# Performance work log

Measured on AMD Instinct MI355X. Metric: run time of the kernel, lower is better.

The kernel has to match this reference:

```python
import jax, jax.numpy as jnp
import numpy as np

B, L, D, DFF, MODES = 16, 1536, 512, 2048, 64
KERNELS = (3, 5, 7)


def setup_inputs() -> dict:
    key = jax.random.key(0)
    ks = jax.random.split(key, 12)
    scale = 1.0 / (D * D)
    f32 = jnp.float32
    return {
        "x": jax.random.normal(ks[0], (B, L, D), f32),
        "w_real": scale * jax.random.normal(ks[1], (D, D, MODES), f32),
        "w_imag": scale * jax.random.normal(ks[2], (D, D, MODES), f32),
        "conv1_w": jax.random.normal(ks[3], (DFF, D), f32) / np.sqrt(D).astype(np.float32),
        "conv2_w": jax.random.normal(ks[4], (D, DFF), f32) / np.sqrt(DFF).astype(np.float32),
        "d1_w1": jax.random.normal(ks[5], (D // 2, D), f32) / np.sqrt(D).astype(np.float32),
        "d1_b1": jnp.zeros((D // 2,), f32),
        "d1_w2": jax.random.normal(ks[6], (len(KERNELS), D // 2), f32) / np.sqrt(D // 2).astype(np.float32),
        "d1_b2": jnp.zeros((len(KERNELS),), f32),
        "d2_w1": jax.random.normal(ks[7], (D // 2, D), f32) / np.sqrt(D).astype(np.float32),
        "d2_b1": jnp.zeros((D // 2,), f32),
        "d2_w2": jax.random.normal(ks[8], (len(KERNELS), D // 2), f32) / np.sqrt(D // 2).astype(np.float32),
        "d2_b2": jnp.zeros((len(KERNELS),), f32),
    }


def _avg_pool1d(x, k):
    # torch AvgPool1d(kernel=k, stride=1, padding=k//2), count_include_pad=True:
    # zero-pad then divide by k everywhere. x: (B, L, D) -> (B, L, D) for odd k.
    pad = k // 2
    xp = jnp.pad(x, ((0, 0), (pad, pad), (0, 0)))
    cs = jnp.pad(jnp.cumsum(xp, axis=1), ((0, 0), (1, 0), (0, 0)))
    return (cs[:, k:, :] - cs[:, :-k, :]) / k


def _moe_decomp(x, w1, b1, w2, b2):
    # trends: (B, L, D, E)
    trends = jnp.stack([_avg_pool1d(x, k) for k in KERNELS], axis=-1)
    h = jax.nn.relu(jnp.einsum("bld,hd->blh", x, w1) + b1)
    logits = jnp.einsum("blh,eh->ble", h, w2) + b2
    gates = jax.nn.softmax(logits, axis=-1)[:, :, None, :]  # (B, L, 1, E)
    x_trend = jnp.sum(trends * gates, axis=-1)
    return x - x_trend  # seasonal component


def _fourier_block(x, w_real, w_imag):
    q_ft = jnp.fft.rfft(x, axis=1)  # (B, L//2+1, D) complex
    modes = min(MODES, q_ft.shape[1])
    weights = (w_real + 1j * w_imag).astype(jnp.complex64)  # (D, D, modes)
    # batched complex matmul over the kept modes (fuses the per-mode loop)
    out_m = jnp.einsum("bmd,dem->bme", q_ft[:, :modes, :], weights[:, :, :modes])
    out_ft = jnp.zeros((x.shape[0], x.shape[1] // 2 + 1, x.shape[2]), jnp.complex64)
    out_ft = out_ft.at[:, :modes, :].set(out_m)
    return jnp.fft.irfft(out_ft, n=x.shape[1], axis=1)


def reference(x, w_real, w_imag, conv1_w, conv2_w,
              d1_w1, d1_b1, d1_w2, d1_b2,
              d2_w1, d2_b1, d2_w2, d2_b2):
    # FEB-f + residual (dropout = identity in eval)
    x = x + _fourier_block(x, w_real, w_imag)
    x = _moe_decomp(x, d1_w1, d1_b1, d1_w2, d1_b2)
    # 1x1 conv FFN == per-token linear layers
    y = jax.nn.relu(jnp.einsum("bld,fd->blf", x, conv1_w))
    y = jnp.einsum("blf,df->bld", y, conv2_w)
    res = _moe_decomp(x + y, d2_w1, d2_b1, d2_w2, d2_b2)
    return res
```

## Files before the change

kernel.cpp:

```cpp
#include <hip/hip_runtime.h>

#define B_   16
#define L_   1536
#define D_   512
#define DFF_ 2048
#define NM   64
#define HID  256

typedef short short8  __attribute__((ext_vector_type(8)));
typedef short short4v __attribute__((ext_vector_type(4)));
typedef float f32x4   __attribute__((ext_vector_type(4)));

__device__ __forceinline__ float b2f(short s) {
  unsigned int u = ((unsigned int)(unsigned short)s) << 16;
  float f; __builtin_memcpy(&f, &u, 4); return f;
}
__device__ __forceinline__ short f2b(float f) {
  unsigned int u; __builtin_memcpy(&u, &f, 4);
  u += 0x7fffu + ((u >> 16) & 1u);
  return (short)(u >> 16);
}
__device__ __forceinline__ f32x4 zero4() {
  f32x4 v; v[0]=0.f; v[1]=0.f; v[2]=0.f; v[3]=0.f; return v;
}

#define MFMA(a,b,c) __builtin_amdgcn_mfma_f32_16x16x32_bf16((a),(b),(c),0,0,0)
#define SWZ(row, grp) (((row) << 6) + ((((grp) ^ ((row) & 7))) << 3))
#define GLDS16(gp, lp) __builtin_amdgcn_global_load_lds( \
    (const __attribute__((address_space(1))) void*)(gp), \
    (__attribute__((address_space(3))) void*)(lp), 16, 0, 0)
#define MEMFENCE asm volatile("" ::: "memory")

__global__ __launch_bounds__(256) void zero_out(float* __restrict__ o, int n) {
  int i = blockIdx.x * 256 + threadIdx.x;
  if (i < n) o[i] = 0.f;
}

__global__ __launch_bounds__(256) void prep_all(
    const float* __restrict__ conv1_w, const float* __restrict__ conv2_w,
    const float* __restrict__ d1_w1,  const float* __restrict__ d2_w1,
    short* __restrict__ c1, short* __restrict__ c2,
    short* __restrict__ dw1, short* __restrict__ dw2,
    short* __restrict__ tcs, short* __restrict__ basis)
{
  int blk = blockIdx.x;
  if (blk < 2304) {
    const float* s; short* d; int i;
    if (blk < 1024)      { s = conv1_w; d = c1;  i = blk * 256 + threadIdx.x; }
    else if (blk < 2048) { s = conv2_w; d = c2;  i = (blk - 1024) * 256 + threadIdx.x; }
    else if (blk < 2176) { s = d1_w1;   d = dw1; i = (blk - 2048) * 256 + threadIdx.x; }
    else                 { s = d2_w1;   d = dw2; i = (blk - 2176) * 256 + threadIdx.x; }
    f32x4 v = ((const f32x4*)s)[i];
    short4v o;
    #pragma unroll
    for (int j = 0; j < 4; ++j) o[j] = f2b(v[j]);
    ((short4v*)d)[i] = o;
    return;
  }
  if (blk < 3072) {
    int i = (blk - 2304) * 256 + threadIdx.x;
    int m = i / L_, l = i - m * L_;
    int mm = (m < 64) ? m : (m - 64);
    int r = (mm * l) % L_;
    float th = (float)r * (6.283185307179586f / (float)L_);
    float s, c; __sincosf(th, &s, &c);
    tcs[i] = f2b((m < 64) ? c : -s);
    return;
  }
  {
    int i = (blk - 3072) * 256 + threadIdx.x;
    int l = i >> 7, k = i & 127;
    int m = (k < 64) ? k : (k - 64);
    int r = (m * l) % L_;
    float th = (float)r * (6.283185307179586f / (float)L_);
    float s, c; __sincosf(th, &s, &c);
    float v = (k < 64) ? ((m == 0) ? 1.f : 2.f) * (1.f / (float)L_) * c
                       : (-2.f / (float)L_) * s;
    basis[i] = f2b(v);
  }
}

__global__ __launch_bounds__(256) void transpose_w(
    const float* __restrict__ wre, const float* __restrict__ wim,
    short* __restrict__ wtr, short* __restrict__ wti)
{
  __shared__ float tile[64][17];
  int dc = blockIdx.x, e = blockIdx.y, t = threadIdx.x;
  int zz = blockIdx.z;
  const float* w = (zz < 4) ? wre : wim;
  short* wt      = (zz < 4) ? wtr : wti;
  int mBase = (zz & 3) * 16;
  {
    int dl = t >> 2, mg = t & 3;
    f32x4 v = *(const f32x4*)(w + ((long)(dc * 64 + dl) * 512 + e) * 64 + mBase + mg * 4);
    tile[dl][mg*4+0] = v[0]; tile[dl][mg*4+1] = v[1];
    tile[dl][mg*4+2] = v[2]; tile[dl][mg*4+3] = v[3];
  }
  __syncthreads();
  if (t < 128) {
    int mr = t >> 3, dg = t & 7;
    short8 o;
    #pragma unroll
    for (int j = 0; j < 8; ++j) o[j] = f2b(tile[dg * 8 + j][mr]);
    *(short8*)(wt + ((long)(mBase + mr) * 512 + e) * 512 + dc * 64 + dg * 8) = o;
  }
}

__global__ __launch_bounds__(256) void transpose_x(const float* __restrict__ x,
                                                   short* __restrict__ xt) {
  __shared__ float tile[64][65];
  int dc = blockIdx.x, lc = blockIdx.y, b = blockIdx.z, t = threadIdx.x;
  const float* xb = x + (long)b * L_ * D_;
  #pragma unroll
  for (int i = 0; i < 4; ++i) {
    int idx = i * 256 + t; int ll = idx >> 4, dg = idx & 15;
    f32x4 v = *(const f32x4*)(xb + (long)(lc * 64 + ll) * D_ + dc * 64 + dg * 4);
    tile[ll][dg*4+0] = v[0]; tile[ll][dg*4+1] = v[1];
    tile[ll][dg*4+2] = v[2]; tile[ll][dg*4+3] = v[3];
  }
  __syncthreads();
  #pragma unroll
  for (int i = 0; i < 2; ++i) {
    int idx = i * 256 + t; int dl = idx >> 3, lg = idx & 7;
    short8 o;
    #pragma unroll
    for (int j = 0; j < 8; ++j) o[j] = f2b(tile[lg * 8 + j][dl]);
    *(short8*)(xt + ((long)b * D_ + dc * 64 + dl) * L_ + lc * 64 + lg * 8) = o;
  }
}

template<bool RELU, bool HASBIAS>
__global__ __launch_bounds__(256) void gemm64(
    const short* __restrict__ A, long ldA,
    const short* __restrict__ W, long ldW,
    const float* __restrict__ bias,
    short* __restrict__ outB, long csr, long csc, int K)
{
  __shared__ short lA[2][64 * 64];
  __shared__ short lW[2][64 * 64];
  const int t = threadIdx.x, lane = t & 63, wid = t >> 6;
  const int quad = lane >> 4, l15 = lane & 15;
  const int wm = (wid & 1) * 32, wn = (wid >> 1) * 32;
  const long row0 = (long)blockIdx.x * 64, col0 = (long)blockIdx.y * 64;
  const short* Ab = A + row0 * ldA;
  const short* Wb = W + col0 * ldW;

  int srcrow[2]; long srcoff[2];
  #pragma unroll
  for (int i = 0; i < 2; ++i) {
    int c = wid * 2 + i;
    int r = c * 8 + (lane >> 3);
    int g = (lane & 7) ^ (r & 7);
    srcrow[i] = r; srcoff[i] = g * 8;
  }

  f32x4 acc[2][2];
  #pragma unroll
  for (int i = 0; i < 2; ++i)
    #pragma unroll
    for (int j = 0; j < 2; ++j) acc[i][j] = zero4();

  const int nk = K >> 6;
  #pragma unroll
  for (int i = 0; i < 2; ++i) {
    int c = wid * 2 + i;
    GLDS16(Ab + (long)srcrow[i] * ldA + srcoff[i], lA[0] + c * 512);
    GLDS16(Wb + (long)srcrow[i] * ldW + srcoff[i], lW[0] + c * 512);
  }
  if (nk > 1) {
    #pragma unroll
    for (int i = 0; i < 2; ++i) {
      int c = wid * 2 + i;
      GLDS16(Ab + (long)srcrow[i] * ldA + 64 + srcoff[i], lA[1] + c * 512);
      GLDS16(Wb + (long)srcrow[i] * ldW + 64 + srcoff[i], lW[1] + c * 512);
    }
  }

  for (int it = 0; it < nk; ++it) {
    if (it + 1 < nk) asm volatile("s_waitcnt vmcnt(4)" ::: "memory");
    else             asm volatile("s_waitcnt vmcnt(0)" ::: "memory");
    __builtin_amdgcn_s_barrier();
    const int cur = it & 1;
    const short* bufA = lA[cur];
    const short* bufW = lW[cur];
    #pragma unroll
    for (int ks = 0; ks < 2; ++ks) {
      int gq = ks * 4 + quad;
      short8 a0 = *(const short8*)&bufA[SWZ(wm + l15, gq)];
      short8 a1 = *(const short8*)&bufA[SWZ(wm + 16 + l15, gq)];
      short8 b0 = *(const short8*)&bufW[SWZ(wn + l15, gq)];
      short8 b1 = *(const short8*)&bufW[SWZ(wn + 16 + l15, gq)];
      acc[0][0] = MFMA(a0, b0, acc[0][0]);
      acc[0][1] = MFMA(a0, b1, acc[0][1]);
      acc[1][0] = MFMA(a1, b0, acc[1][0]);
      acc[1][1] = MFMA(a1, b1, acc[1][1]);
    }
    asm volatile("s_waitcnt lgkmcnt(0)" ::: "memory");
    __builtin_amdgcn_s_barrier();
    const long kn = (long)(it + 2) * 64;
    if (kn < K) {
      #pragma unroll
      for (int i = 0; i < 2; ++i) {
        int c = wid * 2 + i;
        GLDS16(Ab + (long)srcrow[i] * ldA + kn + srcoff[i], lA[cur] + c * 512);
        GLDS16(Wb + (long)srcrow[i] * ldW + kn + srcoff[i], lW[cur] + c * 512);
      }
    }
  }

  #pragma unroll
  for (int ni = 0; ni < 2; ++ni) {
    long col = col0 + wn + ni * 16 + l15;
    float bvv = HASBIAS ? bias[col] : 0.f;
    #pragma unroll
    for (int mi = 0; mi < 2; ++mi) {
      #pragma unroll
      for (int r = 0; r < 4; ++r) {
        long row = row0 + wm + mi * 16 + quad * 4 + r;
        float v = acc[mi][ni][r];
        if (HASBIAS) v += bvv;
        if (RELU)    v = fmaxf(v, 0.f);
        outB[row * csr + col * csc] = f2b(v);
      }
    }
  }
}

template<bool RELU, bool HASBIAS, bool HASRES, bool RESB>
__global__ __launch_bounds__(256) void gemm128(
    const short* __restrict__ A, long ldA, long Az,
    const short* __restrict__ W, long ldW, long Wz,
    const float* __restrict__ bias,
    const void* __restrict__ res, long ldres, long resZ,
    short* __restrict__ outB, long ldC, long Cz, int K)
{
  __shared__ short lA[2][128 * 64];
  __shared__ short lW[2][128 * 64];
  const int t = threadIdx.x, lane = t & 63, wid = t >> 6;
  const int quad = lane >> 4, l15 = lane & 15;
  const int wm = (wid & 1) * 64, wn = (wid >> 1) * 64;
  const long row0 = (long)blockIdx.x * 128, col0 = (long)blockIdx.y * 128;
  const int z = blockIdx.z;
  const short* Ab = A + (long)z * Az + row0 * ldA;
  const short* Wb = W + (long)z * Wz + col0 * ldW;

  int srcrow[4]; long srcoff[4];
  #pragma unroll
  for (int i = 0; i < 4; ++i) {
    int c = wid * 4 + i;
    int r = c * 8 + (lane >> 3);
    int g = (lane & 7) ^ (r & 7);
    srcrow[i] = r; srcoff[i] = g * 8;
  }

  f32x4 acc[4][4];
  #pragma unroll
  for (int i = 0; i < 4; ++i)
    #pragma unroll
    for (int j = 0; j < 4; ++j) acc[i][j] = zero4();

  const int nk = K >> 6;
  #pragma unroll
  for (int i = 0; i < 4; ++i) {
    int c = wid * 4 + i;
    GLDS16(Ab + (long)srcrow[i] * ldA + srcoff[i], lA[0] + c * 512);
    GLDS16(Wb + (long)srcrow[i] * ldW + srcoff[i], lW[0] + c * 512);
  }
  if (nk > 1) {
    #pragma unroll
    for (int i = 0; i < 4; ++i) {
      int c = wid * 4 + i;
      GLDS16(Ab + (long)srcrow[i] * ldA + 64 + srcoff[i], lA[1] + c * 512);
      GLDS16(Wb + (long)srcrow[i] * ldW + 64 + srcoff[i], lW[1] + c * 512);
    }
  }

  for (int it = 0; it < nk; ++it) {
    if (it + 1 < nk) asm volatile("s_waitcnt vmcnt(8)" ::: "memory");
    else             asm volatile("s_waitcnt vmcnt(0)" ::: "memory");
    __builtin_amdgcn_s_barrier();
    const int cur = it & 1;
    const short* bufA = lA[cur];
    const short* bufW = lW[cur];
    #pragma unroll
    for (int ks = 0; ks < 2; ++ks) {
      int gq = ks * 4 + quad;
      short8 av[4], bv[4];
      #pragma unroll
      for (int mi = 0; mi < 4; ++mi) av[mi] = *(const short8*)&bufA[SWZ(wm + mi * 16 + l15, gq)];
      #pragma unroll
      for (int ni = 0; ni < 4; ++ni) bv[ni] = *(const short8*)&bufW[SWZ(wn + ni * 16 + l15, gq)];
      #pragma unroll
      for (int mi = 0; mi < 4; ++mi)
        #pragma unroll
        for (int ni = 0; ni < 4; ++ni)
          acc[mi][ni] = MFMA(av[mi], bv[ni], acc[mi][ni]);
    }
    asm volatile("s_waitcnt lgkmcnt(0)" ::: "memory");
    __builtin_amdgcn_s_barrier();
    const long kn = (long)(it + 2) * 64;
    if (kn < K) {
      #pragma unroll
      for (int i = 0; i < 4; ++i) {
        int c = wid * 4 + i;
        GLDS16(Ab + (long)srcrow[i] * ldA + kn + srcoff[i], lA[cur] + c * 512);
        GLDS16(Wb + (long)srcrow[i] * ldW + kn + srcoff[i], lW[cur] + c * 512);
      }
    }
  }

  #pragma unroll
  for (int ni = 0; ni < 4; ++ni) {
    long col = col0 + wn + ni * 16 + l15;
    float bvv = HASBIAS ? bias[col] : 0.f;
    #pragma unroll
    for (int mi = 0; mi < 4; ++mi) {
      #pragma unroll
      for (int r = 0; r < 4; ++r) {
        long row = row0 + wm + mi * 16 + quad * 4 + r;
        float v = acc[mi][ni][r];
        if (HASBIAS) v += bvv;
        if (RELU)    v = fmaxf(v, 0.f);
        if (HASRES) {
          long ro = (long)z * resZ + row * ldres + col;
          v += RESB ? b2f(((const short*)res)[ro]) : ((const float*)res)[ro];
        }
        outB[(long)z * Cz + row * ldC + col] = f2b(v);
      }
    }
  }
}

template<bool RELU, bool HASRES>
__global__ __launch_bounds__(512, 2) void gemm256(
    const short* __restrict__ A, long ldA,
    const short* __restrict__ W, long ldW,
    const short* __restrict__ res, long ldres,
    short* __restrict__ outB, long ldC, int K, int gn)
{
  __shared__ short sh[65536];
  const int t = threadIdx.x;
  const int lane = t & 63, wid = t >> 6;
  const int quad = lane >> 4, l15 = lane & 15;
  const int wr = wid >> 2, wc = wid & 3;
  const int wch = wc >> 1, cbw = (wc & 1) * 64;

  const int nwg = gridDim.x;
  const int cpx = nwg >> 3;
  const int wg = (blockIdx.x & 7) * cpx + (blockIdx.x >> 3);
  const int bx = wg / gn, by = wg - bx * gn;
  const long row0 = (long)bx * 256, col0 = (long)by * 256;

  const short* Ab = A + row0 * ldA;
  const short* Wb = W + col0 * ldW;

  const int srw = t >> 3;
  const int sg  = (t & 7) ^ (srw & 7);

#define STAGE(TP, KB) do {                                                   \
    const long ko_ = (long)(KB) + sg * 8;                                    \
    _Pragma("unroll")                                                        \
    for (int h_ = 0; h_ < 2; ++h_) {                                         \
      short* dA_ = sh + ((TP) * 2 + h_) * 8192;                              \
      short* dB_ = sh + 32768 + ((TP) * 2 + h_) * 8192;                      \
      _Pragma("unroll")                                                      \
      for (int j_ = 0; j_ < 2; ++j_) {                                       \
        const long gr_ = (long)(h_ * 128 + srw + j_ * 64);                   \
        GLDS16(Ab + gr_ * ldA + ko_, dA_ + (j_ * 512 + t) * 8);              \
        GLDS16(Wb + gr_ * ldW + ko_, dB_ + (j_ * 512 + t) * 8);              \
      }                                                                      \
    }                                                                        \
  } while (0)

  f32x4 acc[8][4];
  #pragma unroll
  for (int i = 0; i < 8; ++i)
    #pragma unroll
    for (int j = 0; j < 4; ++j) acc[i][j] = zero4();

#define PH_LOADS(TP, QM, QN)                                                 \
    const short* aS_ = sh + ((TP) * 2 + wr) * 8192;                          \
    const short* bS_ = sh + 32768 + ((TP) * 2 + wch) * 8192;                 \
    short8 av[4][2], bv[2][2];                                               \
    _Pragma("unroll")                                                        \
    for (int u = 0; u < 4; ++u)                                              \
      _Pragma("unroll")                                                      \
      for (int ks = 0; ks < 2; ++ks)                                         \
        av[u][ks] = *(const short8*)&aS_[SWZ(((QM)*4+u)*16 + l15, ks*4 + quad)]; \
    _Pragma("unroll")                                                        \
    for (int v = 0; v < 2; ++v)                                              \
      _Pragma("unroll")                                                      \
      for (int ks = 0; ks < 2; ++ks)                                         \
        bv[v][ks] = *(const short8*)&bS_[SWZ(cbw + ((QN)*2+v)*16 + l15, ks*4 + quad)];

#define PH_MMA(QM, QN) do {                                                  \
    asm volatile("s_waitcnt lgkmcnt(0)" ::: "memory");                       \
    __builtin_amdgcn_s_setprio(1);                                           \
    _Pragma("unroll")                                                        \
    for (int ks = 0; ks < 2; ++ks)                                           \
      _Pragma("unroll")                                                      \
      for (int u = 0; u < 4; ++u)                                            \
        _Pragma("unroll")                                                    \
        for (int v = 0; v < 2; ++v)                                          \
          acc[(QM)*4+u][(QN)*2+v] =                                          \
              MFMA(av[u][ks], bv[v][ks], acc[(QM)*4+u][(QN)*2+v]);           \
    __builtin_amdgcn_s_setprio(0);                                           \
  } while (0)

#define PH_LEAD(TP, QM, QN) do {                                             \
    PH_LOADS(TP, QM, QN);                                                    \
    PH_MMA(QM, QN);                                                          \
    MEMFENCE; __builtin_amdgcn_s_barrier(); MEMFENCE;                        \
  } while (0)

#define PH_MID(TP, QM, QN) do {                                              \
    PH_LOADS(TP, QM, QN);                                                    \
    MEMFENCE; __builtin_amdgcn_s_barrier();                                  \
    PH_MMA(QM, QN);                                                          \
    MEMFENCE; __builtin_amdgcn_s_barrier(); MEMFENCE;                        \
  } while (0)

  const int NI = K >> 7;
  STAGE(0, 0);

  for (int i = 0; i < NI; ++i) {
    const int kb = i << 7;
    STAGE(1, kb + 64);
    asm volatile("s_waitcnt vmcnt(8)" ::: "memory");
    __builtin_amdgcn_s_barrier(); MEMFENCE;
    PH_LEAD(0, 0, 0);
    PH_MID(0, 1, 0);
    PH_MID(0, 0, 1);
    PH_MID(0, 1, 1);
    if (i + 1 < NI) {
      STAGE(0, kb + 128);
      asm volatile("s_waitcnt vmcnt(8)" ::: "memory");
    } else {
      asm volatile("s_waitcnt vmcnt(0)" ::: "memory");
    }
    __builtin_amdgcn_s_barrier(); MEMFENCE;
    PH_LEAD(1, 0, 0);
    PH_MID(1, 1, 0);
    PH_MID(1, 0, 1);
    PH_MID(1, 1, 1);
  }

  #pragma unroll
  for (int ni = 0; ni < 4; ++ni) {
    long col = col0 + wc * 64 + ni * 16 + l15;
    #pragma unroll
    for (int mi = 0; mi < 8; ++mi) {
      #pragma unroll
      for (int r = 0; r < 4; ++r) {
        long row = row0 + wr * 128 + mi * 16 + quad * 4 + r;
        float v = acc[mi][ni][r];
        if (RELU) v = fmaxf(v, 0.f);
        if (HASRES) v += b2f(res[row * ldres + col]);
        outB[row * ldC + col] = f2b(v);
      }
    }
  }
#undef STAGE
#undef PH_LOADS
#undef PH_MMA
#undef PH_LEAD
#undef PH_MID
}

__global__ __launch_bounds__(256) void mode_gemm(
    const short* __restrict__ qr, const short* __restrict__ qi,
    const short* __restrict__ wr, const short* __restrict__ wi,
    short* __restrict__ outm)
{
  __shared__ short lqr[16 * 64], lqi[16 * 64], lwr[64 * 64], lwi[64 * 64];
  const int m = blockIdx.x, en = blockIdx.y;
  const int t = threadIdx.x, lane = t & 63, wid = t >> 6;
  const int quad = lane >> 4, l15 = lane & 15;
  const short* qrb = qr + (long)m * (B_ * D_);
  const short* qib = qi + (long)m * (B_ * D_);
  const short* wrb = wr + (long)m * (D_ * D_) + (long)en * 64 * D_;
  const short* wib = wi + (long)m * (D_ * D_) + (long)en * 64 * D_;
  f32x4 accr = zero4(), acci = zero4();
  for (int k0 = 0; k0 < D_; k0 += 64) {
    __syncthreads();
    {
      int idx = t & 127; int r = idx >> 3, cg = idx & 7;
      const short* src = (t < 128 ? qrb : qib) + r * D_ + k0 + cg * 8;
      short* dst = (t < 128) ? lqr : lqi;
      *(short8*)&dst[SWZ(r, cg)] = *(const short8*)src;
    }
    #pragma unroll
    for (int i = 0; i < 4; ++i) {
      int idx = i * 256 + t;
      int which = idx >> 9, idx2 = idx & 511;
      int r = idx2 >> 3, cg = idx2 & 7;
      const short* src = (which ? wib : wrb) + r * D_ + k0 + cg * 8;
      short* dst = which ? lwi : lwr;
      *(short8*)&dst[SWZ(r, cg)] = *(const short8*)src;
    }
    __syncthreads();
    #pragma unroll
    for (int ks = 0; ks < 2; ++ks) {
      int gq = ks * 4 + quad;
      short8 ar = *(const short8*)&lqr[SWZ(l15, gq)];
      short8 ai = *(const short8*)&lqi[SWZ(l15, gq)];
      short8 br = *(const short8*)&lwr[SWZ(wid * 16 + l15, gq)];
      short8 bi = *(const short8*)&lwi[SWZ(wid * 16 + l15, gq)];
      short8 nai;
      #pragma unroll
      for (int j = 0; j < 8; ++j) nai[j] = (short)(ai[j] ^ (short)0x8000);
      accr = MFMA(ar, br, accr);
      accr = MFMA(nai, bi, accr);
      acci = MFMA(ar, bi, acci);
      acci = MFMA(ai, br, acci);
    }
  }
  #pragma unroll
  for (int r = 0; r < 4; ++r) {
    int bb = quad * 4 + r;
    long e = (long)en * 64 + wid * 16 + l15;
    long base = ((long)bb * D_ + e) * 128 + m;
    outm[base]      = f2b(accr[r]);
    outm[base + 64] = f2b(acci[r]);
  }
}

template<bool OUTF, bool WRITEB>
__global__ __launch_bounds__(512) void combine_kernel(
    const short* __restrict__ xin, const short* __restrict__ h,
    const float* __restrict__ w2, const float* __restrict__ b2,
    float* __restrict__ outf, short* __restrict__ outb)
{
  __shared__ float lG[64][4];
  int lc = blockIdx.x, b = blockIdx.y, t = threadIdx.x;
  int wid = t >> 6, lane = t & 63;
  int l0 = lc * 64;
  #pragma unroll
  for (int pi = 0; pi < 8; ++pi) {
    int pos = wid * 8 + pi;
    long row = (long)b * L_ + l0 + pos;
    short4v hh = *(const short4v*)(h + row * HID + lane * 4);
    float hv[4];
    #pragma unroll
    for (int j = 0; j < 4; ++j) hv[j] = b2f(hh[j]);
    float lg[3];
    #pragma unroll
    for (int e = 0; e < 3; ++e) {
      const float* wrow = w2 + e * HID + lane * 4;
      float p = hv[0] * wrow[0] + hv[1] * wrow[1] + hv[2] * wrow[2] + hv[3] * wrow[3];
      #pragma unroll
      for (int off = 32; off >= 1; off >>= 1) p += __shfl_xor(p, off);
      lg[e] = p + b2[e];
    }
    float mx = fmaxf(lg[0], fmaxf(lg[1], lg[2]));
    float e0 = __expf(lg[0] - mx), e1 = __expf(lg[1] - mx), e2 = __expf(lg[2] - mx);
    float inv = 1.f / (e0 + e1 + e2);
    float gv = (lane == 0) ? e0 * inv : (lane == 1) ? e1 * inv : e2 * inv;
    if (lane < 3) lG[pos][lane] = gv;
  }
  __syncthreads();

  int d = t;
  const short* xb = xin + (long)b * L_ * D_ + d;
  float win[7];
  #pragma unroll
  for (int j = 0; j < 6; ++j) {
    int l = l0 - 3 + j;
    win[j] = (l >= 0 && l < L_) ? b2f(xb[(long)l * D_]) : 0.f;
  }
  for (int i = 0; i < 64; ++i) {
    int lcn = l0 + i;
    int lr = lcn + 3;
    win[6] = (lr < L_) ? b2f(xb[(long)lr * D_]) : 0.f;
    float s3 = win[2] + win[3] + win[4];
    float s5 = s3 + win[1] + win[5];
    float s7 = s5 + win[0] + win[6];
    float trend = lG[i][0] * s3 * (1.f / 3.f) + lG[i][1] * s5 * (1.f / 5.f)
                + lG[i][2] * s7 * (1.f / 7.f);
    float v = win[3] - trend;
    long o = ((long)b * L_ + lcn) * D_ + d;
    if (OUTF)   outf[o] = v;
    if (WRITEB) outb[o] = f2b(v);
    #pragma unroll
    for (int j = 0; j < 6; ++j) win[j] = win[j + 1];
  }
}

extern "C" void kernel_launch(void* const* d_in, const int* in_sizes, int n_in,
                              void* d_out, int out_size, void* d_ws, size_t ws_size,
                              hipStream_t stream) {
  const float* x       = (const float*)d_in[0];
  const float* w_real  = (const float*)d_in[1];
  const float* w_imag  = (const float*)d_in[2];
  const float* conv1_w = (const float*)d_in[3];
  const float* conv2_w = (const float*)d_in[4];
  const float* d1_w1   = (const float*)d_in[5];
  const float* d1_b1   = (const float*)d_in[6];
  const float* d1_w2   = (const float*)d_in[7];
  const float* d1_b2   = (const float*)d_in[8];
  const float* d2_w1   = (const float*)d_in[9];
  const float* d2_b1   = (const float*)d_in[10];
  const float* d2_w2   = (const float*)d_in[11];
  const float* d2_b2   = (const float*)d_in[12];
  float* OUT = (float*)d_out;

  const size_t REQ_BIG = 144703488, REQ_SMALL = 98566144;
  if (ws_size < REQ_SMALL) {
    zero_out<<<(out_size + 255) / 256, 256, 0, stream>>>(OUT, out_size);
    return;
  }
  const bool big = (ws_size >= REQ_BIG);

  char* ws = (char*)d_ws;
  short* C1WB  = (short*)(ws + 0);
  short* C2WB  = (short*)(ws + 2097152);
  short* D1W1B = (short*)(ws + 4194304);
  short* D2W1B = (short*)(ws + 4456448);
  short* TCS   = (short*)(ws + 4718592);
  short* BASIS = (short*)(ws + 5111808);
  short* XT    = (short*)(ws + 6291456);
  short* Y1    = XT;
  short* QRI   = (short*)(ws + 31457280);
  short* OUTM  = (short*)(ws + 33554432);
  short* WTR   = (short*)(ws + 35651584);
  short* X1B   = WTR;
  short* WTI   = (short*)(ws + 69206016);
  short* X2B   = (short*)(ws + (big ? 106954752 : 60817408));
  short* H     = (short*)(ws + (big ? 132120576 : 85983232));

  prep_all<<<3840, 256, 0, stream>>>(conv1_w, conv2_w, d1_w1, d2_w1,
                                     C1WB, C2WB, D1W1B, D2W1B, TCS, BASIS);
  transpose_w<<<dim3(8, 512, 8), 256, 0, stream>>>(w_real, w_imag, WTR, WTI);
  transpose_x<<<dim3(8, 24, 16), 256, 0, stream>>>(x, XT);

  gemm64<false, false><<<dim3(128, 2), 256, 0, stream>>>(
      XT, L_, TCS, L_, nullptr, QRI, 1, (long)B_ * D_, L_);

  mode_gemm<<<dim3(64, 8), 256, 0, stream>>>(QRI, QRI + 64 * B_ * D_, WTR, WTI, OUTM);

  gemm128<false, false, true, false><<<dim3(12, 4, 16), 256, 0, stream>>>(
      BASIS, 128, 0, OUTM, 128, (long)D_ * 128, nullptr,
      x, D_, (long)L_ * D_, X1B, D_, (long)L_ * D_, 128);

  gemm64<true, true><<<dim3(384, 4), 256, 0, stream>>>(
      X1B, D_, D1W1B, D_, d1_b1, H, HID, 1, D_);
  combine_kernel<false, true><<<dim3(24, 16), 512, 0, stream>>>(
      X1B, H, d1_w2, d1_b2, nullptr, X2B);

  {
    const int nchunk = big ? 1 : 2;
    const long rows = big ? 24576 : 12288;
    const int gm = (int)(rows / 256);
    for (int rc = 0; rc < nchunk; ++rc) {
      short* Ain = X2B + (long)rc * rows * D_;
      gemm256<true, false><<<dim3(gm * (DFF_ / 256)), 512, 0, stream>>>(
          Ain, D_, C1WB, D_, nullptr, 0, Y1, DFF_, D_, DFF_ / 256);
      gemm256<false, true><<<dim3(gm * (D_ / 256)), 512, 0, stream>>>(
          Y1, DFF_, C2WB, DFF_, Ain, D_, Ain, D_, DFF_, D_ / 256);
    }
  }

  gemm64<true, true><<<dim3(384, 4), 256, 0, stream>>>(
      X2B, D_, D2W1B, D_, d2_b1, H, HID, 1, D_);
  combine_kernel<true, false><<<dim3(24, 16), 512, 0, stream>>>(
      X2B, H, d2_w2, d2_b2, OUT, nullptr);
}
```

Before: 586.5 us.

## Restructure GEMM main loop to per-64K-step double buffering with inline-asm LDS reads

Replaces the four-phase-per-tile GEMM inner loop, which used many block barriers, with one iteration per 64-wide K slice. Each iteration issues all LDS fragment reads up front with raw ds_read_b128 and precomputed swizzled addresses, then runs MFMAs on the first half of the A rows while the second half's reads are still in flight. Barrier count per K step drops sharply and LDS reads overlap with matrix math. In exchange it holds more fragment registers live at once, which may pressure occupancy, and it depends on manual lgkmcnt counting for correctness.

Result: no change. 582.9 us (-0.6%).

```diff
diff --git a/kernel.cpp b/kernel.cpp
--- a/kernel.cpp
+++ b/kernel.cpp
@@ -30,6 +30,15 @@
     (const __attribute__((address_space(1))) void*)(gp), \
     (__attribute__((address_space(3))) void*)(lp), 16, 0, 0)
 #define MEMFENCE asm volatile("" ::: "memory")
+
+__device__ __forceinline__ unsigned ldsaddr(const void* p) {
+  return (unsigned)(unsigned long long)(const __attribute__((address_space(3))) void*)p;
+}
+__device__ __forceinline__ short8 dsr128(unsigned a) {
+  short8 r;
+  asm volatile("ds_read_b128 %0, %1" : "=v"(r) : "v"(a));
+  return r;
+}
 
 __global__ __launch_bounds__(256) void zero_out(float* __restrict__ o, int n) {
   int i = blockIdx.x * 256 + threadIdx.x;
@@ -345,12 +354,10 @@
   const int wr = wid >> 2, wc = wid & 3;
   const int wch = wc >> 1, cbw = (wc & 1) * 64;
 
-  const int nwg = gridDim.x;
-  const int cpx = nwg >> 3;
+  const int nwg = gridDim.x, cpx = nwg >> 3;
   const int wg = (blockIdx.x & 7) * cpx + (blockIdx.x >> 3);
   const int bx = wg / gn, by = wg - bx * gn;
   const long row0 = (long)bx * 256, col0 = (long)by * 256;
-
   const short* Ab = A + row0 * ldA;
   const short* Wb = W + col0 * ldW;
 
@@ -372,77 +379,72 @@
     }                                                                        \
   } while (0)
 
+  const unsigned shb  = ldsaddr(sh);
+  const unsigned swz0 = (unsigned)((quad ^ (l15 & 7)) << 4);
+  const unsigned swz1 = swz0 ^ 64u;
+  const unsigned aB = shb + wr * 16384u + (unsigned)(l15 * 128);
+  const unsigned bB = shb + 65536u + wch * 16384u + (unsigned)((cbw + l15) * 128);
+
   f32x4 acc[8][4];
   #pragma unroll
   for (int i = 0; i < 8; ++i)
     #pragma unroll
     for (int j = 0; j < 4; ++j) acc[i][j] = zero4();
 
-#define PH_LOADS(TP, QM, QN)                                                 \
-    const short* aS_ = sh + ((TP) * 2 + wr) * 8192;                          \
-    const short* bS_ = sh + 32768 + ((TP) * 2 + wch) * 8192;                 \
-    short8 av[4][2], bv[2][2];                                               \
-    _Pragma("unroll")                                                        \
-    for (int u = 0; u < 4; ++u)                                              \
-      _Pragma("unroll")                                                      \
-      for (int ks = 0; ks < 2; ++ks)                                         \
-        av[u][ks] = *(const short8*)&aS_[SWZ(((QM)*4+u)*16 + l15, ks*4 + quad)]; \
-    _Pragma("unroll")                                                        \
-    for (int v = 0; v < 2; ++v)                                              \
-      _Pragma("unroll")                                                      \
-      for (int ks = 0; ks < 2; ++ks)                                         \
-        bv[v][ks] = *(const short8*)&bS_[SWZ(cbw + ((QN)*2+v)*16 + l15, ks*4 + quad)];
-
-#define PH_MMA(QM, QN) do {                                                  \
-    asm volatile("s_waitcnt lgkmcnt(0)" ::: "memory");                       \
-    __builtin_amdgcn_s_setprio(1);                                           \
-    _Pragma("unroll")                                                        \
-    for (int ks = 0; ks < 2; ++ks)                                           \
-      _Pragma("unroll")                                                      \
-      for (int u = 0; u < 4; ++u)                                            \
-        _Pragma("unroll")                                                    \
-        for (int v = 0; v < 2; ++v)                                          \
-          acc[(QM)*4+u][(QN)*2+v] =                                          \
-              MFMA(av[u][ks], bv[v][ks], acc[(QM)*4+u][(QN)*2+v]);           \
-    __builtin_amdgcn_s_setprio(0);                                           \
-  } while (0)
-
-#define PH_LEAD(TP, QM, QN) do {                                             \
-    PH_LOADS(TP, QM, QN);                                                    \
-    PH_MMA(QM, QN);                                                          \
-    MEMFENCE; __builtin_amdgcn_s_barrier(); MEMFENCE;                        \
-  } while (0)
-
-#define PH_MID(TP, QM, QN) do {                                              \
-    PH_LOADS(TP, QM, QN);                                                    \
-    MEMFENCE; __builtin_amdgcn_s_barrier();                                  \
-    PH_MMA(QM, QN);                                                          \
-    MEMFENCE; __builtin_amdgcn_s_barrier(); MEMFENCE;                        \
-  } while (0)
-
-  const int NI = K >> 7;
+  const int NK = K >> 6;
   STAGE(0, 0);
 
-  for (int i = 0; i < NI; ++i) {
-    const int kb = i << 7;
-    STAGE(1, kb + 64);
-    asm volatile("s_waitcnt vmcnt(8)" ::: "memory");
-    __builtin_amdgcn_s_barrier(); MEMFENCE;
-    PH_LEAD(0, 0, 0);
-    PH_MID(0, 1, 0);
-    PH_MID(0, 0, 1);
-    PH_MID(0, 1, 1);
-    if (i + 1 < NI) {
-      STAGE(0, kb + 128);
+  for (int i = 0; i < NK; ++i) {
+    const unsigned tpo = (unsigned)(i & 1) * 32768u;
+    if (i + 1 < NK) {
+      STAGE((i + 1) & 1, (i + 1) << 6);
       asm volatile("s_waitcnt vmcnt(8)" ::: "memory");
     } else {
       asm volatile("s_waitcnt vmcnt(0)" ::: "memory");
     }
-    __builtin_amdgcn_s_barrier(); MEMFENCE;
-    PH_LEAD(1, 0, 0);
-    PH_MID(1, 1, 0);
-    PH_MID(1, 0, 1);
-    PH_MID(1, 1, 1);
+    __builtin_amdgcn_s_barrier();
+    __builtin_amdgcn_sched_barrier(0);
+
+    short8 bv[4][2], a0[4][2], a1[4][2];
+    #pragma unroll
+    for (int ni = 0; ni < 4; ++ni) {
+      bv[ni][0] = dsr128(bB + tpo + ni * 2048u + swz0);
+      bv[ni][1] = dsr128(bB + tpo + ni * 2048u + swz1);
+    }
+    #pragma unroll
+    for (int u = 0; u < 4; ++u) {
+      a0[u][0] = dsr128(aB + tpo + u * 2048u + swz0);
+      a0[u][1] = dsr128(aB + tpo + u * 2048u + swz1);
+    }
+    #pragma unroll
+    for (int u = 0; u < 4; ++u) {
+      a1[u][0] = dsr128(aB + tpo + 8192u + u * 2048u + swz0);
+      a1[u][1] = dsr128(aB + tpo + 8192u + u * 2048u + swz1);
+    }
+    asm volatile("s_waitcnt lgkmcnt(8)" ::: "memory");
+    __builtin_amdgcn_sched_barrier(0);
+    __builtin_amdgcn_s_setprio(1);
+    #pragma unroll
+    for (int ks = 0; ks < 2; ++ks)
+      #pragma unroll
+      for (int u = 0; u < 4; ++u)
+        #pragma unroll
+        for (int ni = 0; ni < 4; ++ni)
+          acc[u][ni] = MFMA(a0[u][ks], bv[ni][ks], acc[u][ni]);
+    __builtin_amdgcn_s_setprio(0);
+    asm volatile("s_waitcnt lgkmcnt(0)" ::: "memory");
+    __builtin_amdgcn_sched_barrier(0);
+    __builtin_amdgcn_s_setprio(1);
+    #pragma unroll
+    for (int ks = 0; ks < 2; ++ks)
+      #pragma unroll
+      for (int u = 0; u < 4; ++u)
+        #pragma unroll
+        for (int ni = 0; ni < 4; ++ni)
+          acc[4 + u][ni] = MFMA(a1[u][ks], bv[ni][ks], acc[4 + u][ni]);
+    __builtin_amdgcn_s_setprio(0);
+    __builtin_amdgcn_sched_barrier(0);
+    __builtin_amdgcn_s_barrier();
   }
 
   #pragma unroll
@@ -461,10 +463,6 @@
     }
   }
 #undef STAGE
-#undef PH_LOADS
-#undef PH_MMA
-#undef PH_LEAD
-#undef PH_MID
 }
 
 __global__ __launch_bounds__(256) void mode_gemm(
```
